# Kernel tuning notes

Measured on AMD Instinct MI355X. Metric: run time of the kernel, lower is better.

## Reference

```python
import jax, jax.numpy as jnp
import numpy as np

N_NODES = 50000
N_EDGES = 800000
D_IN = 128
D_HID = 128
D_OUT = 128


def _sage_conv(x, edge_index, Wp, bp, Wl, bl, Wr):
    """PyG SAGEConv with project=True, mean aggregation, root weight, bias.

    x: [N, d_in]; edge_index: [2, E] (row 0 = src j, row 1 = dst i).
    out = mean_j relu(x_j @ Wp.T + bp) @ Wl.T + bl + x_i @ Wr.T
    """
    src, dst = edge_index[0], edge_index[1]
    n = x.shape[0]
    h = jax.nn.relu(x @ Wp.T + bp)          # [N, d_in] projected neighbor feats
    msg = h[src]                             # [E, d_in] gather
    agg_sum = jax.ops.segment_sum(msg, dst, num_segments=n)          # [N, d_in]
    cnt = jax.ops.segment_sum(jnp.ones((msg.shape[0],), x.dtype), dst,
                              num_segments=n)                        # [N]
    agg = agg_sum / jnp.maximum(cnt, 1.0)[:, None]                   # mean
    return agg @ Wl.T + bl + x @ Wr.T


def setup_inputs() -> dict:
    key = jax.random.key(0)
    ks = jax.random.split(key, 12)
    s = lambda d: 1.0 / np.sqrt(d)
    x = jax.random.normal(ks[0], (N_NODES, D_IN), dtype=jnp.float32)
    edge_index = jax.random.randint(ks[1], (2, N_EDGES), 0, N_NODES, dtype=jnp.int64)
    return {
        "x": x,
        "edge_index": edge_index,
        # layer 1
        "Wp1": jax.random.normal(ks[2], (D_IN, D_IN), jnp.float32) * s(D_IN),
        "bp1": jnp.zeros((D_IN,), jnp.float32),
        "Wl1": jax.random.normal(ks[3], (D_HID, D_IN), jnp.float32) * s(D_IN),
        "bl1": jnp.zeros((D_HID,), jnp.float32),
        "Wr1": jax.random.normal(ks[4], (D_HID, D_IN), jnp.float32) * s(D_IN),
        # layer 2
        "Wp2": jax.random.normal(ks[5], (D_HID, D_HID), jnp.float32) * s(D_HID),
        "bp2": jnp.zeros((D_HID,), jnp.float32),
        "Wl2": jax.random.normal(ks[6], (D_OUT, D_HID), jnp.float32) * s(D_HID),
        "bl2": jnp.zeros((D_OUT,), jnp.float32),
        "Wr2": jax.random.normal(ks[7], (D_OUT, D_HID), jnp.float32) * s(D_HID),
    }


def reference(x, edge_index, Wp1, bp1, Wl1, bl1, Wr1, Wp2, bp2, Wl2, bl2, Wr2):
    h = jax.nn.relu(_sage_conv(x, edge_index, Wp1, bp1, Wl1, bl1, Wr1))
    out = _sage_conv(h, edge_index, Wp2, bp2, Wl2, bl2, Wr2)
    return out
```

## Files before the change

kernel.cpp:

```cpp
#include <hip/hip_runtime.h>

#define NN 50000
#define NE 800000
#define D 128
#define NTILE 3128
#define GGRID 768
#define XBLK 6250
#define WBLK 96
#define BBLK 1000
#define EPB 800
#define NBUCK 49
#define STAGE_CAP 64
#define BIN_CAP 20480
#define SORT_WIN 18432

typedef __attribute__((ext_vector_type(8))) short bf16x8;
typedef __attribute__((ext_vector_type(4))) float f32x4;

__device__ inline unsigned short f2bf(float f) {
    union { float f; unsigned u; } v; v.f = f;
    unsigned r = v.u + 0x7FFF + ((v.u >> 16) & 1);
    return (unsigned short)(r >> 16);
}
__device__ inline float bf2f(unsigned b) {
    union { unsigned u; float f; } v; v.u = b << 16;
    return v.f;
}

__global__ __launch_bounds__(256)
void prep(const float* __restrict__ x,
          const float* __restrict__ w0, const float* __restrict__ w1,
          const float* __restrict__ w2, const float* __restrict__ w3,
          const float* __restrict__ w4, const float* __restrict__ w5,
          const int* __restrict__ ei,
          unsigned short* __restrict__ xb, unsigned short* __restrict__ wb,
          unsigned* __restrict__ bin, int* __restrict__ bcur) {
    const unsigned b = blockIdx.x;
    if (b < XBLK) {
        int i = b * 256 + threadIdx.x;
        float4 v = ((const float4*)x)[i];
        ushort4 o = {f2bf(v.x), f2bf(v.y), f2bf(v.z), f2bf(v.w)};
        ((ushort4*)xb)[i] = o;
    } else if (b < XBLK + WBLK) {
        const float* ws_[6] = {w0, w1, w2, w3, w4, w5};
        int wi = (int)(b - XBLK) >> 4;
        int off = ((int)(b - XBLK) & 15) * 256 + threadIdx.x;
        float4 v = ((const float4*)ws_[wi])[off];
        ushort4 o = {f2bf(v.x), f2bf(v.y), f2bf(v.z), f2bf(v.w)};
        ((ushort4*)(wb + wi * D * D))[off] = o;
    } else {
        __shared__ unsigned stage[NBUCK * STAGE_CAP];
        __shared__ int bcnt[NBUCK];
        __shared__ int sbase[NBUCK];
        const int ebase = (int)(b - XBLK - WBLK) * EPB;
        if (threadIdx.x < NBUCK) bcnt[threadIdx.x] = 0;
        __syncthreads();
        for (int j = threadIdx.x; j < EPB; j += 256) {
            const int e = ebase + j;
            const int dst = ei[NE + e];
            const int src = ei[e];
            const int bk = dst >> 10;
            const unsigned u = (unsigned)src | ((unsigned)(dst & 1023) << 16);
            const int slot = atomicAdd(&bcnt[bk], 1);
            if (slot < STAGE_CAP) {
                stage[bk * STAGE_CAP + slot] = u;
            } else {
                const int gp = atomicAdd(&bcur[bk], 1);
                bin[bk * BIN_CAP + gp] = u;
            }
        }
        __syncthreads();
        if (threadIdx.x < NBUCK) {
            int c = bcnt[threadIdx.x];
            if (c > STAGE_CAP) c = STAGE_CAP;
            sbase[threadIdx.x] = atomicAdd(&bcur[threadIdx.x], c);
        }
        __syncthreads();
        const int wv = threadIdx.x >> 6, ln = threadIdx.x & 63;
        for (int bk = wv; bk < NBUCK; bk += 4) {
            int c = bcnt[bk];
            if (c > STAGE_CAP) c = STAGE_CAP;
            if (ln < c)
                bin[bk * BIN_CAP + sbase[bk] + ln] = stage[bk * STAGE_CAP + ln];
        }
    }
}

__global__ __launch_bounds__(64)
void bucket_scan(const int* __restrict__ bcur, int* __restrict__ bbase,
                 int* __restrict__ row_start) {
    __shared__ int tmp[64];
    int v = (threadIdx.x < NBUCK) ? bcur[threadIdx.x] : 0;
    tmp[threadIdx.x] = v;
    __syncthreads();
    for (int off = 1; off < 64; off <<= 1) {
        int t = (threadIdx.x >= (unsigned)off) ? tmp[threadIdx.x - off] : 0;
        __syncthreads();
        tmp[threadIdx.x] += t;
        __syncthreads();
    }
    if (threadIdx.x <= NBUCK)
        bbase[threadIdx.x] = (threadIdx.x == 0) ? 0 : tmp[threadIdx.x - 1];
    if (threadIdx.x == 0) row_start[NN] = NE;
}

template <typename OUTT, bool DUAL>
__device__ inline void gemm_body(const unsigned short* __restrict__ A1,
                                 const unsigned short* __restrict__ W1,
                                 const unsigned short* __restrict__ A2,
                                 const unsigned short* __restrict__ W2,
                                 const float* __restrict__ bias,
                                 OUTT* __restrict__ out, int do_relu,
                                 int bid, int nblk) {
    const int lane = threadIdx.x & 63;
    const int wave = threadIdx.x >> 6;
    const int quad = lane >> 4;
    const int l16 = lane & 15;
    const int c0 = wave * 32 + l16;
    const int c1 = c0 + 16;

    const float bv0 = bias[c0];
    const float bv1 = bias[c1];

    bf16x8 w10[4], w11[4], w20[4], w21[4];
#pragma unroll
    for (int kt = 0; kt < 4; ++kt) {
        const int ko = kt * 32 + quad * 8;
        w10[kt] = *(const bf16x8*)&W1[c0 * D + ko];
        w11[kt] = *(const bf16x8*)&W1[c1 * D + ko];
        if (DUAL) {
            w20[kt] = *(const bf16x8*)&W2[c0 * D + ko];
            w21[kt] = *(const bf16x8*)&W2[c1 * D + ko];
        }
    }

    for (int t = bid; t < NTILE; t += nblk) {
        const int row0 = t * 16;
        int r = row0 + l16;
        const int arow = (r < NN ? r : NN - 1) * D;

        f32x4 acc0 = (f32x4){0.f, 0.f, 0.f, 0.f};
        f32x4 acc1 = (f32x4){0.f, 0.f, 0.f, 0.f};
#pragma unroll
        for (int kt = 0; kt < 4; ++kt) {
            const int ko = kt * 32 + quad * 8;
            bf16x8 a1 = *(const bf16x8*)&A1[arow + ko];
            acc0 = __builtin_amdgcn_mfma_f32_16x16x32_bf16(a1, w10[kt], acc0, 0, 0, 0);
            acc1 = __builtin_amdgcn_mfma_f32_16x16x32_bf16(a1, w11[kt], acc1, 0, 0, 0);
            if (DUAL) {
                bf16x8 a2 = *(const bf16x8*)&A2[arow + ko];
                acc0 = __builtin_amdgcn_mfma_f32_16x16x32_bf16(a2, w20[kt], acc0, 0, 0, 0);
                acc1 = __builtin_amdgcn_mfma_f32_16x16x32_bf16(a2, w21[kt], acc1, 0, 0, 0);
            }
        }

#pragma unroll
        for (int rr = 0; rr < 4; ++rr) {
            const int row = row0 + quad * 4 + rr;
            if (row < NN) {
                float v0 = acc0[rr] + bv0;
                float v1 = acc1[rr] + bv1;
                if (do_relu) {
                    v0 = v0 > 0.f ? v0 : 0.f;
                    v1 = v1 > 0.f ? v1 : 0.f;
                }
                if constexpr (sizeof(OUTT) == 2) {
                    out[row * D + c0] = (OUTT)f2bf(v0);
                    out[row * D + c1] = (OUTT)f2bf(v1);
                } else {
                    out[row * D + c0] = (OUTT)v0;
                    out[row * D + c1] = (OUTT)v1;
                }
            }
        }
    }
}

template <typename OUTT, bool DUAL>
__global__ __launch_bounds__(256)
void gemm_persist(const unsigned short* __restrict__ A1,
                  const unsigned short* __restrict__ W1,
                  const unsigned short* __restrict__ A2,
                  const unsigned short* __restrict__ W2,
                  const float* __restrict__ bias, OUTT* __restrict__ out,
                  int do_relu) {
    gemm_body<OUTT, DUAL>(A1, W1, A2, W2, bias, out, do_relu, blockIdx.x, GGRID);
}

__global__ __launch_bounds__(256)
void gemm_fill(const unsigned short* __restrict__ A,
               const unsigned short* __restrict__ W,
               const float* __restrict__ bias, unsigned short* __restrict__ outp,
               const int* __restrict__ bbase, const unsigned* __restrict__ bin,
               int* __restrict__ row_start, unsigned short* __restrict__ src16) {
    if (blockIdx.x < GGRID) {
        gemm_body<unsigned short, false>(A, W, nullptr, nullptr, bias, outp, 1,
                                         blockIdx.x, GGRID);
        return;
    }
    __shared__ int hist[1024];
    __shared__ int tsum[256];
    __shared__ unsigned short win[SORT_WIN];
    const int b = (int)blockIdx.x - GGRID;
    const int nbase = b << 10;
    const int nn = (NN - nbase < 1024) ? (NN - nbase) : 1024;
    const int gb = bbase[b];
    const int span = bbase[b + 1] - gb;
    const unsigned* mybin = bin + (size_t)b * BIN_CAP;

    for (int i = threadIdx.x; i < 1024; i += 256) hist[i] = 0;
    __syncthreads();
    for (int i = threadIdx.x; i < span; i += 256)
        atomicAdd(&hist[mybin[i] >> 16], 1);
    __syncthreads();

    int h[4], s = 0;
#pragma unroll
    for (int j = 0; j < 4; ++j) {
        h[j] = hist[threadIdx.x * 4 + j];
        s += h[j];
    }
    tsum[threadIdx.x] = s;
    __syncthreads();
    for (int off = 1; off < 256; off <<= 1) {
        int t = (threadIdx.x >= (unsigned)off) ? tsum[threadIdx.x - off] : 0;
        __syncthreads();
        tsum[threadIdx.x] += t;
        __syncthreads();
    }
    int ex = tsum[threadIdx.x] - s;
#pragma unroll
    for (int j = 0; j < 4; ++j) {
        const int idx = threadIdx.x * 4 + j;
        hist[idx] = ex;
        if (idx < nn) row_start[nbase + idx] = gb + ex;
        ex += h[j];
    }
    __syncthreads();

    for (int i = threadIdx.x; i < span; i += 256) {
        const unsigned u = mybin[i];
        const int pos = atomicAdd(&hist[u >> 16], 1);
        const unsigned short sv = (unsigned short)(u & 0xffffu);
        if (pos < SORT_WIN) win[pos] = sv;
        else src16[gb + pos] = sv;
    }
    __syncthreads();
    const int lim = span < SORT_WIN ? span : SORT_WIN;
    for (int i = threadIdx.x; i < lim; i += 256) src16[gb + i] = win[i];
}

__device__ inline void acc8(float* s, uint4 r) {
    s[0] += bf2f(r.x & 0xffffu); s[1] += bf2f(r.x >> 16);
    s[2] += bf2f(r.y & 0xffffu); s[3] += bf2f(r.y >> 16);
    s[4] += bf2f(r.z & 0xffffu); s[5] += bf2f(r.z >> 16);
    s[6] += bf2f(r.w & 0xffffu); s[7] += bf2f(r.w >> 16);
}

__global__ __launch_bounds__(256)
void gather_mean4(const uint4* __restrict__ P4, const int* __restrict__ row_start,
                  const unsigned short* __restrict__ src16,
                  uint4* __restrict__ agg4) {
    const int n = blockIdx.x * 4 + (threadIdx.x >> 6);
    const int lane = threadIdx.x & 63;
    const int q = lane >> 4;
    const int l16 = lane & 15;
    const int b = row_start[n];
    const int e = row_start[n + 1];

    float s[8];
#pragma unroll
    for (int j = 0; j < 8; ++j) s[j] = 0.f;

    int i = b;
    for (; i + 16 <= e; i += 16) {
        int i0 = src16[i + 0 + q];
        int i1 = src16[i + 4 + q];
        int i2 = src16[i + 8 + q];
        int i3 = src16[i + 12 + q];
        uint4 r0 = P4[i0 * 16 + l16];
        uint4 r1 = P4[i1 * 16 + l16];
        uint4 r2 = P4[i2 * 16 + l16];
        uint4 r3 = P4[i3 * 16 + l16];
        acc8(s, r0); acc8(s, r1); acc8(s, r2); acc8(s, r3);
    }
    for (; i + 4 <= e; i += 4) {
        int i0 = src16[i + q];
        uint4 r0 = P4[i0 * 16 + l16];
        acc8(s, r0);
    }
    const int rem = e - i;
    if (q < rem) {
        int i0 = src16[i + q];
        uint4 r0 = P4[i0 * 16 + l16];
        acc8(s, r0);
    }

#pragma unroll
    for (int j = 0; j < 8; ++j) {
        s[j] += __shfl_xor(s[j], 16);
        s[j] += __shfl_xor(s[j], 32);
    }

    const int deg = e - b;
    const float inv = 1.0f / (float)(deg > 0 ? deg : 1);
    if (q == 0) {
        uint4 o;
        o.x = (unsigned)f2bf(s[0] * inv) | ((unsigned)f2bf(s[1] * inv) << 16);
        o.y = (unsigned)f2bf(s[2] * inv) | ((unsigned)f2bf(s[3] * inv) << 16);
        o.z = (unsigned)f2bf(s[4] * inv) | ((unsigned)f2bf(s[5] * inv) << 16);
        o.w = (unsigned)f2bf(s[6] * inv) | ((unsigned)f2bf(s[7] * inv) << 16);
        agg4[n * 16 + l16] = o;
    }
}

extern "C" void kernel_launch(void* const* d_in, const int* in_sizes, int n_in,
                              void* d_out, int out_size, void* d_ws, size_t ws_size,
                              hipStream_t stream) {
    const float* x   = (const float*)d_in[0];
    const int*   ei  = (const int*)d_in[1];
    const float* Wp1 = (const float*)d_in[2];
    const float* bp1 = (const float*)d_in[3];
    const float* Wl1 = (const float*)d_in[4];
    const float* bl1 = (const float*)d_in[5];
    const float* Wr1 = (const float*)d_in[6];
    const float* Wp2 = (const float*)d_in[7];
    const float* bp2 = (const float*)d_in[8];
    const float* Wl2 = (const float*)d_in[9];
    const float* bl2 = (const float*)d_in[10];
    const float* Wr2 = (const float*)d_in[11];
    float* out = (float*)d_out;

    char* ws = (char*)d_ws;
    size_t off = 0;
    auto alloc = [&](size_t bytes) {
        void* p = ws + off;
        off += (bytes + 511) & ~511ull;
        return p;
    };
    unsigned short* Wb   = (unsigned short*)alloc((size_t)6 * D * D * 2);
    unsigned short* xb   = (unsigned short*)alloc((size_t)NN * D * 2);
    unsigned short* bufP = (unsigned short*)alloc((size_t)NN * D * 2);
    unsigned short* bufAg= (unsigned short*)alloc((size_t)NN * D * 2);
    unsigned short* bufH = (unsigned short*)alloc((size_t)NN * D * 2);
    int* row_start  = (int*)alloc((size_t)(NN + 1) * 4);
    int* bcur       = (int*)alloc((size_t)NBUCK * 4);
    int* bbase      = (int*)alloc((size_t)(NBUCK + 1) * 4);
    unsigned* bin   = (unsigned*)alloc((size_t)NBUCK * BIN_CAP * 4);
    unsigned short* src16 = (unsigned short*)alloc((size_t)NE * 2);

    hipMemsetAsync(bcur, 0, (size_t)NBUCK * 4, stream);
    prep<<<XBLK + WBLK + BBLK, 256, 0, stream>>>(
        x, Wp1, Wl1, Wr1, Wp2, Wl2, Wr2, ei, xb, Wb, bin, bcur);

    bucket_scan<<<1, 64, 0, stream>>>(bcur, bbase, row_start);

    gemm_fill<<<GGRID + NBUCK, 256, 0, stream>>>(
        xb, Wb + 0 * D * D, bp1, bufP, bbase, bin, row_start, src16);

    const int GA = NN / 4;

    gather_mean4<<<GA, 256, 0, stream>>>(
        (const uint4*)bufP, row_start, src16, (uint4*)bufAg);
    gemm_persist<unsigned short, true><<<GGRID, 256, 0, stream>>>(
        bufAg, Wb + 1 * D * D, xb, Wb + 2 * D * D, bl1, bufH, 1);

    gemm_persist<unsigned short, false><<<GGRID, 256, 0, stream>>>(
        bufH, Wb + 3 * D * D, nullptr, nullptr, bp2, bufP, 1);

    gather_mean4<<<GA, 256, 0, stream>>>(
        (const uint4*)bufP, row_start, src16, (uint4*)bufAg);
    gemm_persist<float, true><<<GGRID, 256, 0, stream>>>(
        bufAg, Wb + 4 * D * D, bufH, Wb + 5 * D * D, bl2, out, 0);
}
```

Before: 274.9 us.

## Fuse layer-1 combine with layer-2 projection; finer dst buckets; deeper gather unroll

Replaces the two back-to-back GEMM launches (layer-1 combine and layer-2 projection) with one kernel. It computes relu(agg@Wl+x@Wr+b) per 16-row tile, stages the result in shared memory and immediately applies the Wp2 projection, so bufH does not have to be re-read from global memory. The edge bucketing moves from 49 buckets of 1024 nodes to 196 buckets of 256 nodes, which shrinks the per-bucket sort and scan work and gives the CSR build more parallel blocks. The gather loop gets an 8-way unrolled path to keep more loads in flight. The smaller BIN_CAP now silently drops edges if a bucket overflows, which risks wrong results on skewed graphs.

Result: faster. 248.8 us (-9.5%).

```diff
diff --git a/kernel.cpp b/kernel.cpp
--- a/kernel.cpp
+++ b/kernel.cpp
@@ -7,12 +7,13 @@
 #define GGRID 768
 #define XBLK 6250
 #define WBLK 96
-#define BBLK 1000
-#define EPB 800
-#define NBUCK 49
+#define BBLK 250
+#define EPB 3200
+#define NBUCK 196
 #define STAGE_CAP 64
-#define BIN_CAP 20480
-#define SORT_WIN 18432
+#define BIN_CAP 4608
+#define SORT_WIN 4608
+#define LDS_STRIDE 136
 
 typedef __attribute__((ext_vector_type(8))) short bf16x8;
 typedef __attribute__((ext_vector_type(4))) float f32x4;
@@ -59,14 +60,14 @@
             const int e = ebase + j;
             const int dst = ei[NE + e];
             const int src = ei[e];
-            const int bk = dst >> 10;
-            const unsigned u = (unsigned)src | ((unsigned)(dst & 1023) << 16);
+            const int bk = dst >> 8;
+            const unsigned u = (unsigned)src | ((unsigned)(dst & 255) << 16);
             const int slot = atomicAdd(&bcnt[bk], 1);
             if (slot < STAGE_CAP) {
                 stage[bk * STAGE_CAP + slot] = u;
             } else {
                 const int gp = atomicAdd(&bcur[bk], 1);
-                bin[bk * BIN_CAP + gp] = u;
+                if (gp < BIN_CAP) bin[bk * BIN_CAP + gp] = u;
             }
         }
         __syncthreads();
@@ -80,20 +81,22 @@
         for (int bk = wv; bk < NBUCK; bk += 4) {
             int c = bcnt[bk];
             if (c > STAGE_CAP) c = STAGE_CAP;
-            if (ln < c)
-                bin[bk * BIN_CAP + sbase[bk] + ln] = stage[bk * STAGE_CAP + ln];
-        }
-    }
-}
-
-__global__ __launch_bounds__(64)
+            if (ln < c) {
+                int p = sbase[bk] + ln;
+                if (p < BIN_CAP) bin[bk * BIN_CAP + p] = stage[bk * STAGE_CAP + ln];
+            }
+        }
+    }
+}
+
+__global__ __launch_bounds__(256)
 void bucket_scan(const int* __restrict__ bcur, int* __restrict__ bbase,
                  int* __restrict__ row_start) {
-    __shared__ int tmp[64];
+    __shared__ int tmp[256];
     int v = (threadIdx.x < NBUCK) ? bcur[threadIdx.x] : 0;
     tmp[threadIdx.x] = v;
     __syncthreads();
-    for (int off = 1; off < 64; off <<= 1) {
+    for (int off = 1; off < 256; off <<= 1) {
         int t = (threadIdx.x >= (unsigned)off) ? tmp[threadIdx.x - off] : 0;
         __syncthreads();
         tmp[threadIdx.x] += t;
@@ -188,6 +191,96 @@
 }
 
 __global__ __launch_bounds__(256)
+void combine_proj(const unsigned short* __restrict__ Ag,
+                  const unsigned short* __restrict__ Wl,
+                  const unsigned short* __restrict__ X,
+                  const unsigned short* __restrict__ Wr,
+                  const float* __restrict__ bl, unsigned short* __restrict__ bufH,
+                  const unsigned short* __restrict__ Wp,
+                  const float* __restrict__ bp, unsigned short* __restrict__ bufP2) {
+    __shared__ unsigned short tile[16 * LDS_STRIDE];
+    const int lane = threadIdx.x & 63;
+    const int wave = threadIdx.x >> 6;
+    const int quad = lane >> 4;
+    const int l16 = lane & 15;
+    const int c0 = wave * 32 + l16;
+    const int c1 = c0 + 16;
+
+    const float bl0 = bl[c0], bl1 = bl[c1];
+    const float bp0 = bp[c0], bp1 = bp[c1];
+
+    bf16x8 wl0[4], wl1[4], wr0[4], wr1[4];
+#pragma unroll
+    for (int kt = 0; kt < 4; ++kt) {
+        const int ko = kt * 32 + quad * 8;
+        wl0[kt] = *(const bf16x8*)&Wl[c0 * D + ko];
+        wl1[kt] = *(const bf16x8*)&Wl[c1 * D + ko];
+        wr0[kt] = *(const bf16x8*)&Wr[c0 * D + ko];
+        wr1[kt] = *(const bf16x8*)&Wr[c1 * D + ko];
+    }
+
+    for (int t = blockIdx.x; t < NTILE; t += GGRID) {
+        const int row0 = t * 16;
+        int r = row0 + l16;
+        const int arow = (r < NN ? r : NN - 1) * D;
+
+        f32x4 acc0 = (f32x4){0.f, 0.f, 0.f, 0.f};
+        f32x4 acc1 = (f32x4){0.f, 0.f, 0.f, 0.f};
+#pragma unroll
+        for (int kt = 0; kt < 4; ++kt) {
+            const int ko = kt * 32 + quad * 8;
+            bf16x8 a1 = *(const bf16x8*)&Ag[arow + ko];
+            bf16x8 a2 = *(const bf16x8*)&X[arow + ko];
+            acc0 = __builtin_amdgcn_mfma_f32_16x16x32_bf16(a1, wl0[kt], acc0, 0, 0, 0);
+            acc1 = __builtin_amdgcn_mfma_f32_16x16x32_bf16(a1, wl1[kt], acc1, 0, 0, 0);
+            acc0 = __builtin_amdgcn_mfma_f32_16x16x32_bf16(a2, wr0[kt], acc0, 0, 0, 0);
+            acc1 = __builtin_amdgcn_mfma_f32_16x16x32_bf16(a2, wr1[kt], acc1, 0, 0, 0);
+        }
+#pragma unroll
+        for (int rr = 0; rr < 4; ++rr) {
+            const int row = row0 + quad * 4 + rr;
+            float v0 = acc0[rr] + bl0;
+            float v1 = acc1[rr] + bl1;
+            v0 = v0 > 0.f ? v0 : 0.f;
+            v1 = v1 > 0.f ? v1 : 0.f;
+            const unsigned short h0 = f2bf(v0), h1 = f2bf(v1);
+            tile[(quad * 4 + rr) * LDS_STRIDE + c0] = h0;
+            tile[(quad * 4 + rr) * LDS_STRIDE + c1] = h1;
+            if (row < NN) {
+                bufH[row * D + c0] = h0;
+                bufH[row * D + c1] = h1;
+            }
+        }
+        __syncthreads();
+
+        f32x4 p0 = (f32x4){0.f, 0.f, 0.f, 0.f};
+        f32x4 p1 = (f32x4){0.f, 0.f, 0.f, 0.f};
+#pragma unroll
+        for (int kt = 0; kt < 4; ++kt) {
+            const int ko = kt * 32 + quad * 8;
+            bf16x8 aL = *(const bf16x8*)&tile[l16 * LDS_STRIDE + ko];
+            bf16x8 wp0 = *(const bf16x8*)&Wp[c0 * D + ko];
+            bf16x8 wp1 = *(const bf16x8*)&Wp[c1 * D + ko];
+            p0 = __builtin_amdgcn_mfma_f32_16x16x32_bf16(aL, wp0, p0, 0, 0, 0);
+            p1 = __builtin_amdgcn_mfma_f32_16x16x32_bf16(aL, wp1, p1, 0, 0, 0);
+        }
+#pragma unroll
+        for (int rr = 0; rr < 4; ++rr) {
+            const int row = row0 + quad * 4 + rr;
+            if (row < NN) {
+                float v0 = p0[rr] + bp0;
+                float v1 = p1[rr] + bp1;
+                v0 = v0 > 0.f ? v0 : 0.f;
+                v1 = v1 > 0.f ? v1 : 0.f;
+                bufP2[row * D + c0] = f2bf(v0);
+                bufP2[row * D + c1] = f2bf(v1);
+            }
+        }
+        __syncthreads();
+    }
+}
+
+__global__ __launch_bounds__(256)
 void gemm_fill(const unsigned short* __restrict__ A,
                const unsigned short* __restrict__ W,
                const float* __restrict__ bias, unsigned short* __restrict__ outp,
@@ -198,44 +291,35 @@
                                          blockIdx.x, GGRID);
         return;
     }
-    __shared__ int hist[1024];
-    __shared__ int tsum[256];
+    __shared__ int hist[256];
     __shared__ unsigned short win[SORT_WIN];
     const int b = (int)blockIdx.x - GGRID;
-    const int nbase = b << 10;
-    const int nn = (NN - nbase < 1024) ? (NN - nbase) : 1024;
+    const int nbase = b << 8;
+    const int nn = (NN - nbase < 256) ? (NN - nbase) : 256;
     const int gb = bbase[b];
     const int span = bbase[b + 1] - gb;
     const unsigned* mybin = bin + (size_t)b * BIN_CAP;
 
-    for (int i = threadIdx.x; i < 1024; i += 256) hist[i] = 0;
+    hist[threadIdx.x] = 0;
     __syncthreads();
     for (int i = threadIdx.x; i < span; i += 256)
         atomicAdd(&hist[mybin[i] >> 16], 1);
     __syncthreads();
 
-    int h[4], s = 0;
-#pragma unroll
-    for (int j = 0; j < 4; ++j) {
-        h[j] = hist[threadIdx.x * 4 + j];
-        s += h[j];
-    }
-    tsum[threadIdx.x] = s;
+    const int hv = hist[threadIdx.x];
+    __syncthreads();
+    hist[threadIdx.x] = hv;
     __syncthreads();
     for (int off = 1; off < 256; off <<= 1) {
-        int t = (threadIdx.x >= (unsigned)off) ? tsum[threadIdx.x - off] : 0;
-        __syncthreads();
-        tsum[threadIdx.x] += t;
-        __syncthreads();
-    }
-    int ex = tsum[threadIdx.x] - s;
-#pragma unroll
-    for (int j = 0; j < 4; ++j) {
-        const int idx = threadIdx.x * 4 + j;
-        hist[idx] = ex;
-        if (idx < nn) row_start[nbase + idx] = gb + ex;
-        ex += h[j];
-    }
+        int tv = (threadIdx.x >= (unsigned)off) ? hist[threadIdx.x - off] : 0;
+        __syncthreads();
+        hist[threadIdx.x] += tv;
+        __syncthreads();
+    }
+    const int ex = hist[threadIdx.x] - hv;
+    __syncthreads();
+    hist[threadIdx.x] = ex;
+    if ((int)threadIdx.x < nn) row_start[nbase + threadIdx.x] = gb + ex;
     __syncthreads();
 
     for (int i = threadIdx.x; i < span; i += 256) {
@@ -273,11 +357,19 @@
     for (int j = 0; j < 8; ++j) s[j] = 0.f;
 
     int i = b;
+    for (; i + 32 <= e; i += 32) {
+        int idx[8];
+        uint4 r[8];
+#pragma unroll
+        for (int j = 0; j < 8; ++j) idx[j] = src16[i + j * 4 + q];
+#pragma unroll
+        for (int j = 0; j < 8; ++j) r[j] = P4[idx[j] * 16 + l16];
+#pragma unroll
+        for (int j = 0; j < 8; ++j) acc8(s, r[j]);
+    }
     for (; i + 16 <= e; i += 16) {
-        int i0 = src16[i + 0 + q];
-        int i1 = src16[i + 4 + q];
-        int i2 = src16[i + 8 + q];
-        int i3 = src16[i + 12 + q];
+        int i0 = src16[i + 0 + q], i1 = src16[i + 4 + q];
+        int i2 = src16[i + 8 + q], i3 = src16[i + 12 + q];
         uint4 r0 = P4[i0 * 16 + l16];
         uint4 r1 = P4[i1 * 16 + l16];
         uint4 r2 = P4[i2 * 16 + l16];
@@ -353,7 +445,7 @@
     prep<<<XBLK + WBLK + BBLK, 256, 0, stream>>>(
         x, Wp1, Wl1, Wr1, Wp2, Wl2, Wr2, ei, xb, Wb, bin, bcur);
 
-    bucket_scan<<<1, 64, 0, stream>>>(bcur, bbase, row_start);
+    bucket_scan<<<1, 256, 0, stream>>>(bcur, bbase, row_start);
 
     gemm_fill<<<GGRID + NBUCK, 256, 0, stream>>>(
         xb, Wb + 0 * D * D, bp1, bufP, bbase, bin, row_start, src16);
@@ -362,11 +454,9 @@
 
     gather_mean4<<<GA, 256, 0, stream>>>(
         (const uint4*)bufP, row_start, src16, (uint4*)bufAg);
-    gemm_persist<unsigned short, true><<<GGRID, 256, 0, stream>>>(
-        bufAg, Wb + 1 * D * D, xb, Wb + 2 * D * D, bl1, bufH, 1);
-
-    gemm_persist<unsigned short, false><<<GGRID, 256, 0, stream>>>(
-        bufH, Wb + 3 * D * D, nullptr, nullptr, bp2, bufP, 1);
+    combine_proj<<<GGRID, 256, 0, stream>>>(
+        bufAg, Wb + 1 * D * D, xb, Wb + 2 * D * D, bl1, bufH,
+        Wb + 3 * D * D, bp2, bufP);
 
     gather_mean4<<<GA, 256, 0, stream>>>(
         (const uint4*)bufP, row_start, src16, (uint4*)bufAg);
```
